# Kernel optimization log

Hardware: AMD Instinct MI355X
Metric: run time of the kernel (lower is better)

## Reference

```python
import jax, jax.numpy as jnp
import numpy as np

N_HEAD = 16
D_HEAD = 64
ROPE_BASE = 10000.0


def rotate_half(x):
    # interleaved pair rotation: (x0,x1,x2,x3,...) -> (-x1,x0,-x3,x2,...)
    x1 = x[..., ::2]
    x2 = x[..., 1::2]
    return jnp.stack((-x2, x1), axis=-1).reshape(x.shape)


def rope_tables(T, d_head, dtype):
    inv_freq = 1.0 / (ROPE_BASE ** (jnp.arange(0, d_head, 2, dtype=jnp.float32) / d_head))
    t = jnp.arange(T, dtype=jnp.float32)
    freqs = jnp.outer(t, inv_freq)                       # [T, d_head/2]
    emb = jnp.repeat(freqs, 2, axis=-1)                  # [T, d_head]
    return jnp.cos(emb).astype(dtype), jnp.sin(emb).astype(dtype)


def setup_inputs() -> dict:
    key = jax.random.key(0)
    k1, k2, k3 = jax.random.split(key, 3)
    B, T, D = 4, 2048, 1024
    x = jax.random.normal(k1, (B, T, D), dtype=jnp.float32)
    W_attn = jax.random.normal(k2, (D, 3 * D), dtype=jnp.float32) * 0.02
    W_proj = jax.random.normal(k3, (D, D), dtype=jnp.float32) * 0.02
    return {"x": x, "W_attn": W_attn, "W_proj": W_proj}


def reference(x, W_attn, W_proj):
    B, T, D = x.shape
    qkv = x @ W_attn                                      # [B, T, 3D]
    qkv = qkv.reshape(B, T, 3, N_HEAD, D_HEAD).transpose(2, 0, 3, 1, 4)
    q, k, v = qkv[0], qkv[1], qkv[2]                      # [B, H, T, d]

    cos, sin = rope_tables(T, D_HEAD, q.dtype)            # [T, d]
    q = q * cos + rotate_half(q) * sin
    k = k * cos + rotate_half(k) * sin

    scale = 1.0 / jnp.sqrt(jnp.asarray(D_HEAD, dtype=q.dtype))
    att = jnp.einsum('bhqd,bhkd->bhqk', q, k) * scale     # [B, H, T, T]
    causal = jnp.tril(jnp.ones((T, T), dtype=bool))
    att = jnp.where(causal, att, jnp.asarray(-jnp.inf, dtype=att.dtype))
    att = jax.nn.softmax(att, axis=-1)
    y = jnp.einsum('bhqk,bhkd->bhqd', att, v)             # [B, H, T, d]
    y = y.transpose(0, 2, 1, 3).reshape(B, T, D)
    return y @ W_proj
```

## Files before the change

### kernel.cpp

```cpp
#include <hip/hip_runtime.h>
#include <hip/hip_bf16.h>

typedef unsigned short ushort_t;
typedef __attribute__((ext_vector_type(8))) short bf16x8;
typedef __attribute__((ext_vector_type(4))) float f32x4;
typedef __attribute__((ext_vector_type(4))) unsigned short u16x4;

#define DEVI __device__ __forceinline__

#define WAITVM(N) asm volatile("s_waitcnt vmcnt(" #N ")" ::: "memory")
DEVI void bar_raw() { asm volatile("s_barrier" ::: "memory"); }

DEVI ushort_t f2bf(float f) {
  __hip_bfloat16 h = __float2bfloat16(f);
  return __builtin_bit_cast(unsigned short, h);
}

typedef const __attribute__((address_space(1))) void gvoid_t;
typedef __attribute__((address_space(3))) void lvoid_t;

DEVI void gload_lds16(const void* g, void* l) {
  __builtin_amdgcn_global_load_lds((gvoid_t*)g, (lvoid_t*)l, 16, 0, 0);
}

DEVI f32x4 mfma16(bf16x8 a, bf16x8 b, f32x4 c) {
  return __builtin_amdgcn_mfma_f32_16x16x32_bf16(a, b, c, 0, 0, 0);
}

DEVI bf16x8 lds_frag(const ushort_t* base, int row, int k) {
  int ch = (k >> 3) ^ (row & 7);
  return *(const bf16x8*)(base + row * 64 + ch * 8);
}

template <int ROWS>
DEVI void stage_swz(const ushort_t* src, int ld, ushort_t* lds, int wid, int lane) {
#pragma unroll
  for (int i = 0; i < ROWS / 32; ++i) {
    int r = i * 32 + wid * 8 + (lane >> 3);
    int p = lane & 7;
    int cl = p ^ (r & 7);
    gload_lds16(src + (size_t)r * ld + cl * 8, lds + r * 64 + p * 8);
  }
}


__global__ void k_convert(const float* __restrict__ in, ushort_t* __restrict__ out) {
  int i = blockIdx.x * 256 + threadIdx.x;
  float4 v = ((const float4*)in)[i];
  u16x4 o = {f2bf(v.x), f2bf(v.y), f2bf(v.z), f2bf(v.w)};
  ((u16x4*)out)[i] = o;
}

__global__ void k_transpose(const float* __restrict__ in, ushort_t* __restrict__ out,
                            int R, int C) {
  __shared__ ushort_t tile[64][65];
  int r0 = blockIdx.y * 64, c0 = blockIdx.x * 64;
  int t = threadIdx.x;
  int tc = t & 63, tr = t >> 6;
#pragma unroll
  for (int i = 0; i < 16; ++i) {
    int r = i * 4 + tr;
    tile[r][tc] = f2bf(in[(size_t)(r0 + r) * C + c0 + tc]);
  }
  __syncthreads();
#pragma unroll
  for (int i = 0; i < 16; ++i) {
    int c = i * 4 + tr;
    out[(size_t)(c0 + c) * R + r0 + tc] = tile[tc][c];
  }
}

__global__ void k_rope_tab(float* __restrict__ ct, float* __restrict__ st) {
  int idx = blockIdx.x * 256 + threadIdx.x;
  int t = idx >> 5, i = idx & 31;
  float inv = powf(10000.0f, -(float)(2 * i) * (1.0f / 64.0f));
  float fr = (float)t * inv;
  ct[idx] = cosf(fr);
  st[idx] = sinf(fr);
}


__global__ __launch_bounds__(256, 2) void k_gemm_qkv(
    const ushort_t* __restrict__ A, const ushort_t* __restrict__ Bt,
    const float* __restrict__ ct, const float* __restrict__ st,
    ushort_t* __restrict__ Qo, ushort_t* __restrict__ Ko, ushort_t* __restrict__ Vto) {
  __shared__ ushort_t sA[2][128 * 64];
  __shared__ ushort_t sB[2][128 * 64];
  int bid = blockIdx.x;
  int swz = (bid & 7) * 192 + (bid >> 3);
  int bm = swz / 24, bn = swz - bm * 24;
  int wid = threadIdx.x >> 6, lane = threadIdx.x & 63;
  int wm = wid >> 1, wn = wid & 1;
  const ushort_t* Abase = A + (size_t)bm * 128 * 1024;
  const ushort_t* Bbase = Bt + (size_t)bn * 128 * 1024;
  f32x4 acc[4][4] = {};
  stage_swz<128>(Abase, 1024, sA[0], wid, lane);
  stage_swz<128>(Bbase, 1024, sB[0], wid, lane);
  for (int kt = 0; kt < 16; ++kt) {
    int cur = kt & 1;
    if (kt < 15) {
      stage_swz<128>(Abase + (kt + 1) * 64, 1024, sA[cur ^ 1], wid, lane);
      stage_swz<128>(Bbase + (kt + 1) * 64, 1024, sB[cur ^ 1], wid, lane);
      WAITVM(8);
    } else {
      WAITVM(0);
    }
    bar_raw();
#pragma unroll
    for (int kk = 0; kk < 2; ++kk) {
      bf16x8 af[4], bfr[4];
#pragma unroll
      for (int mt = 0; mt < 4; ++mt)
        af[mt] = lds_frag(sA[cur], wm * 64 + mt * 16 + (lane & 15), kk * 32 + (lane >> 4) * 8);
#pragma unroll
      for (int nt = 0; nt < 4; ++nt)
        bfr[nt] = lds_frag(sB[cur], wn * 64 + nt * 16 + (lane & 15), kk * 32 + (lane >> 4) * 8);
#pragma unroll
      for (int mt = 0; mt < 4; ++mt)
#pragma unroll
        for (int nt = 0; nt < 4; ++nt) acc[mt][nt] = mfma16(af[mt], bfr[nt], acc[mt][nt]);
    }
    bar_raw();
  }
  int gm0 = bm * 128 + wm * 64;
  int gn0 = bn * 128 + wn * 64;
#pragma unroll
  for (int mt = 0; mt < 4; ++mt) {
#pragma unroll
    for (int nt = 0; nt < 4; ++nt) {
      f32x4 v = acc[mt][nt];
      int n = gn0 + nt * 16 + (lane & 15);
      int sidx = n >> 10, h = (n >> 6) & 15, d = n & 63;
      if (sidx == 2) {
        int m0r = gm0 + mt * 16 + (lane >> 4) * 4;
        int b = m0r >> 11, tpos = m0r & 2047;
        u16x4 pk = {f2bf(v[0]), f2bf(v[1]), f2bf(v[2]), f2bf(v[3])};
        *(u16x4*)(Vto + (((size_t)b * 16 + h) * 64 + d) * 2048 + tpos) = pk;
      } else {
        ushort_t* dst = (sidx == 0) ? Qo : Ko;
#pragma unroll
        for (int r = 0; r < 4; ++r) {
          float x = v[r];
          float px = __shfl_xor(x, 1);
          int m = gm0 + mt * 16 + (lane >> 4) * 4 + r;
          int b = m >> 11, tpos = m & 2047;
          float c = ct[tpos * 32 + (d >> 1)];
          float s = st[tpos * 32 + (d >> 1)];
          float val = (d & 1) ? (x * c + px * s) : (x * c - px * s);
          if (sidx == 0) val *= 0.18033688011112042f;
          dst[(((size_t)b * 16 + h) * 2048 + tpos) * 64 + d] = f2bf(val);
        }
      }
    }
  }
}


__global__ __launch_bounds__(256, 2) void k_attn(
    const ushort_t* __restrict__ Qg, const ushort_t* __restrict__ Kg,
    const ushort_t* __restrict__ Vtg, ushort_t* __restrict__ Yg) {
  __shared__ ushort_t sK[2][64 * 64];
  __shared__ ushort_t sV[2][64 * 64];
  __shared__ ushort_t sP[4][2][32 * 64];
  int bid = blockIdx.x;
  int wid = threadIdx.x >> 6, lane = threadIdx.x & 63;
  int bh = (bid & 7) * 8 + ((bid >> 3) & 7);
  int ps = bid >> 6;
  const ushort_t* Qb = Qg + (size_t)bh * (2048 * 64);
  const ushort_t* Kb = Kg + (size_t)bh * (2048 * 64);
  const ushort_t* Vb = Vtg + (size_t)bh * (64 * 2048);
  int b = bh >> 4, h = bh & 15;
  const bf16x8 ones = {0x3F80, 0x3F80, 0x3F80, 0x3F80, 0x3F80, 0x3F80, 0x3F80, 0x3F80};

  for (int t = 0; t < 2; ++t) {
    int qs = t ? (15 - ps) : ps;
    int q0 = qs * 128;
    int qw = q0 + wid * 32;
    int jmaxb = (q0 + 127) >> 6;
    int jmaxw = (qw + 31) >> 6;
    bf16x8 qf[2][2];
#pragma unroll
    for (int mt = 0; mt < 2; ++mt)
#pragma unroll
      for (int kk = 0; kk < 2; ++kk)
        qf[mt][kk] = *(const bf16x8*)(Qb + (size_t)(qw + mt * 16 + (lane & 15)) * 64 +
                                      kk * 32 + (lane >> 4) * 8);
    f32x4 o[2][4] = {};
    f32x4 l[2] = {};
    stage_swz<64>(Kb, 64, sK[0], wid, lane);
    stage_swz<64>(Vb, 2048, sV[0], wid, lane);
    for (int j = 0; j <= jmaxb; ++j) {
      int cur = j & 1;
      if (j < jmaxb) {
        stage_swz<64>(Kb + (size_t)(j + 1) * 64 * 64, 64, sK[cur ^ 1], wid, lane);
        stage_swz<64>(Vb + (j + 1) * 64, 2048, sV[cur ^ 1], wid, lane);
        WAITVM(4);
      } else {
        WAITVM(0);
      }
      bar_raw();
      if (j <= jmaxw) {
        ushort_t* sPw = sP[wid][cur];
        f32x4 st[2][4] = {};
#pragma unroll
        for (int kk = 0; kk < 2; ++kk) {
          bf16x8 kf[4];
#pragma unroll
          for (int nt = 0; nt < 4; ++nt)
            kf[nt] = lds_frag(sK[cur], nt * 16 + (lane & 15), kk * 32 + (lane >> 4) * 8);
#pragma unroll
          for (int mt = 0; mt < 2; ++mt)
#pragma unroll
            for (int nt = 0; nt < 4; ++nt)
              st[mt][nt] = mfma16(kf[nt], qf[mt][kk], st[mt][nt]);
        }
        if (j == jmaxw) {
#pragma unroll
          for (int mt = 0; mt < 2; ++mt)
#pragma unroll
            for (int nt = 0; nt < 4; ++nt)
#pragma unroll
              for (int r = 0; r < 4; ++r) {
                int kv = j * 64 + nt * 16 + (lane >> 4) * 4 + r;
                int q = qw + mt * 16 + (lane & 15);
                if (kv > q) st[mt][nt][r] = -1e30f;
              }
        }
        int g = lane >> 4;
#pragma unroll
        for (int mt = 0; mt < 2; ++mt) {
          int row = mt * 16 + (lane & 15);
#pragma unroll
          for (int nt = 0; nt < 4; ++nt) {
            u16x4 pk = {f2bf(__builtin_amdgcn_exp2f(st[mt][nt][0])),
                        f2bf(__builtin_amdgcn_exp2f(st[mt][nt][1])),
                        f2bf(__builtin_amdgcn_exp2f(st[mt][nt][2])),
                        f2bf(__builtin_amdgcn_exp2f(st[mt][nt][3]))};
            int ch = (nt * 2 + (g >> 1)) ^ (row & 7);
            *(u16x4*)(sPw + row * 64 + ch * 8 + (g & 1) * 4) = pk;
          }
        }
#pragma unroll
        for (int kk = 0; kk < 2; ++kk) {
          bf16x8 pf[2], vf[4];
#pragma unroll
          for (int mt = 0; mt < 2; ++mt)
            pf[mt] = lds_frag(sPw, mt * 16 + (lane & 15), kk * 32 + (lane >> 4) * 8);
#pragma unroll
          for (int dt = 0; dt < 4; ++dt)
            vf[dt] = lds_frag(sV[cur], dt * 16 + (lane & 15), kk * 32 + (lane >> 4) * 8);
#pragma unroll
          for (int mt = 0; mt < 2; ++mt) {
#pragma unroll
            for (int dt = 0; dt < 4; ++dt) o[mt][dt] = mfma16(pf[mt], vf[dt], o[mt][dt]);
            l[mt] = mfma16(pf[mt], ones, l[mt]);
          }
        }
      }
      bar_raw();
    }
#pragma unroll
    for (int mt = 0; mt < 2; ++mt)
#pragma unroll
      for (int r = 0; r < 4; ++r) {
        float inv = 1.0f / l[mt][r];
        int q = qw + mt * 16 + (lane >> 4) * 4 + r;
#pragma unroll
        for (int dt = 0; dt < 4; ++dt) {
          int d = dt * 16 + (lane & 15);
          Yg[((size_t)b * 2048 + q) * 1024 + h * 64 + d] = f2bf(o[mt][dt][r] * inv);
        }
      }
  }
}


__global__ __launch_bounds__(256, 2) void k_gemm_proj(
    const ushort_t* __restrict__ A, const ushort_t* __restrict__ Bt,
    float* __restrict__ out) {
  __shared__ ushort_t sA[2][128 * 64];
  __shared__ ushort_t sB[2][128 * 64];
  int bid = blockIdx.x;
  int swz = (bid & 7) * 64 + (bid >> 3);
  int bm = swz >> 3, bn = swz & 7;
  int wid = threadIdx.x >> 6, lane = threadIdx.x & 63;
  int wm = wid >> 1, wn = wid & 1;
  const ushort_t* Abase = A + (size_t)bm * 128 * 1024;
  const ushort_t* Bbase = Bt + (size_t)bn * 128 * 1024;
  f32x4 acc[4][4] = {};
  stage_swz<128>(Abase, 1024, sA[0], wid, lane);
  stage_swz<128>(Bbase, 1024, sB[0], wid, lane);
  for (int kt = 0; kt < 16; ++kt) {
    int cur = kt & 1;
    if (kt < 15) {
      stage_swz<128>(Abase + (kt + 1) * 64, 1024, sA[cur ^ 1], wid, lane);
      stage_swz<128>(Bbase + (kt + 1) * 64, 1024, sB[cur ^ 1], wid, lane);
      WAITVM(8);
    } else {
      WAITVM(0);
    }
    bar_raw();
#pragma unroll
    for (int kk = 0; kk < 2; ++kk) {
      bf16x8 af[4], bfr[4];
#pragma unroll
      for (int mt = 0; mt < 4; ++mt)
        af[mt] = lds_frag(sA[cur], wm * 64 + mt * 16 + (lane & 15), kk * 32 + (lane >> 4) * 8);
#pragma unroll
      for (int nt = 0; nt < 4; ++nt)
        bfr[nt] = lds_frag(sB[cur], wn * 64 + nt * 16 + (lane & 15), kk * 32 + (lane >> 4) * 8);
#pragma unroll
      for (int mt = 0; mt < 4; ++mt)
#pragma unroll
        for (int nt = 0; nt < 4; ++nt) acc[mt][nt] = mfma16(af[mt], bfr[nt], acc[mt][nt]);
    }
    bar_raw();
  }
  int gm0 = bm * 128 + wm * 64;
  int gn0 = bn * 128 + wn * 64;
#pragma unroll
  for (int mt = 0; mt < 4; ++mt)
#pragma unroll
    for (int nt = 0; nt < 4; ++nt) {
      f32x4 v = acc[mt][nt];
      int n = gn0 + nt * 16 + (lane & 15);
#pragma unroll
      for (int r = 0; r < 4; ++r) {
        int m = gm0 + mt * 16 + (lane >> 4) * 4 + r;
        out[(size_t)m * 1024 + n] = v[r];
      }
    }
}


extern "C" void kernel_launch(void* const* d_in, const int* in_sizes, int n_in,
                              void* d_out, int out_size, void* d_ws, size_t ws_size,
                              hipStream_t stream) {
  (void)in_sizes; (void)n_in; (void)out_size; (void)ws_size;
  const float* x  = (const float*)d_in[0];
  const float* Wa = (const float*)d_in[1];
  const float* Wp = (const float*)d_in[2];
  float* out = (float*)d_out;
  char* ws = (char*)d_ws;

  ushort_t* xb   = (ushort_t*)(ws + 0);
  ushort_t* WaT  = (ushort_t*)(ws + 16777216);
  ushort_t* WpT  = (ushort_t*)(ws + 23068672);
  float*    ctab = (float*)   (ws + 25165824);
  float*    stab = (float*)   (ws + 25427968);
  ushort_t* Qb   = (ushort_t*)(ws + 25690112);
  ushort_t* Kb   = (ushort_t*)(ws + 42467328);
  ushort_t* Vtb  = (ushort_t*)(ws + 59244544);

  k_convert<<<8192, 256, 0, stream>>>(x, xb);
  k_transpose<<<dim3(48, 16), 256, 0, stream>>>(Wa, WaT, 1024, 3072);
  k_transpose<<<dim3(16, 16), 256, 0, stream>>>(Wp, WpT, 1024, 1024);
  k_rope_tab<<<256, 256, 0, stream>>>(ctab, stab);
  k_gemm_qkv<<<1536, 256, 0, stream>>>(xb, WaT, ctab, stab, Qb, Kb, Vtb);
  k_attn<<<512, 256, 0, stream>>>(Qb, Kb, Vtb, xb);
  k_gemm_proj<<<512, 256, 0, stream>>>(xb, WpT, out);
}
```

Baseline: 159.7 us.

## Enlarge GEMM tiles to 512-thread blocks and prioritize MFMA waves in attention

The QKV GEMM grows from 128x128 to 256x256 tiles with 8 waves, and the projection GEMM goes to 256x128 tiles with 512 threads, so each staged tile feeds more MFMAs and global traffic per FLOP drops. The staging helper is generalized to any thread count. The attention kernel raises wave priority around its MFMA sections with s_setprio. The larger tiles use 64KB (QKV) and 48KB (projection) of LDS plus more accumulators per thread, which may lower occupancy. The grids also shrink to 384 and 256 blocks, which may underfill the 256 CUs.

```diff
diff --git a/kernel.cpp b/kernel.cpp
--- a/kernel.cpp
+++ b/kernel.cpp
@@ -32,12 +32,12 @@
   return *(const bf16x8*)(base + row * 64 + ch * 8);
 }
 
-template <int ROWS>
-DEVI void stage_swz(const ushort_t* src, int ld, ushort_t* lds, int wid, int lane) {
-#pragma unroll
-  for (int i = 0; i < ROWS / 32; ++i) {
-    int r = i * 32 + wid * 8 + (lane >> 3);
-    int p = lane & 7;
+template <int ROWS, int THR>
+DEVI void stage_swz(const ushort_t* src, int ld, ushort_t* lds, int tid) {
+#pragma unroll
+  for (int i = 0; i < ROWS / (THR / 8); ++i) {
+    int r = i * (THR / 8) + (tid >> 3);
+    int p = tid & 7;
     int cl = p ^ (r & 7);
     gload_lds16(src + (size_t)r * ld + cl * 8, lds + r * 64 + p * 8);
   }
@@ -80,27 +80,28 @@
 }
 
 
-__global__ __launch_bounds__(256, 2) void k_gemm_qkv(
+__global__ __launch_bounds__(512, 2) void k_gemm_qkv(
     const ushort_t* __restrict__ A, const ushort_t* __restrict__ Bt,
     const float* __restrict__ ct, const float* __restrict__ st,
     ushort_t* __restrict__ Qo, ushort_t* __restrict__ Ko, ushort_t* __restrict__ Vto) {
-  __shared__ ushort_t sA[2][128 * 64];
-  __shared__ ushort_t sB[2][128 * 64];
+  __shared__ ushort_t sA[2][256 * 64];
+  __shared__ ushort_t sB[2][256 * 64];
+  int tid = threadIdx.x;
   int bid = blockIdx.x;
-  int swz = (bid & 7) * 192 + (bid >> 3);
-  int bm = swz / 24, bn = swz - bm * 24;
-  int wid = threadIdx.x >> 6, lane = threadIdx.x & 63;
-  int wm = wid >> 1, wn = wid & 1;
-  const ushort_t* Abase = A + (size_t)bm * 128 * 1024;
-  const ushort_t* Bbase = Bt + (size_t)bn * 128 * 1024;
-  f32x4 acc[4][4] = {};
-  stage_swz<128>(Abase, 1024, sA[0], wid, lane);
-  stage_swz<128>(Bbase, 1024, sB[0], wid, lane);
+  int swz = (bid & 7) * 48 + (bid >> 3);
+  int bm = swz / 12, bn = swz % 12;
+  int lane = tid & 63;
+  int wm = (tid >> 6) >> 2, wn = (tid >> 6) & 3;
+  const ushort_t* Abase = A + (size_t)bm * 256 * 1024;
+  const ushort_t* Bbase = Bt + (size_t)bn * 256 * 1024;
+  f32x4 acc[8][4] = {};
+  stage_swz<256, 512>(Abase, 1024, sA[0], tid);
+  stage_swz<256, 512>(Bbase, 1024, sB[0], tid);
   for (int kt = 0; kt < 16; ++kt) {
     int cur = kt & 1;
     if (kt < 15) {
-      stage_swz<128>(Abase + (kt + 1) * 64, 1024, sA[cur ^ 1], wid, lane);
-      stage_swz<128>(Bbase + (kt + 1) * 64, 1024, sB[cur ^ 1], wid, lane);
+      stage_swz<256, 512>(Abase + (kt + 1) * 64, 1024, sA[cur ^ 1], tid);
+      stage_swz<256, 512>(Bbase + (kt + 1) * 64, 1024, sB[cur ^ 1], tid);
       WAITVM(8);
     } else {
       WAITVM(0);
@@ -108,24 +109,24 @@
     bar_raw();
 #pragma unroll
     for (int kk = 0; kk < 2; ++kk) {
-      bf16x8 af[4], bfr[4];
-#pragma unroll
-      for (int mt = 0; mt < 4; ++mt)
-        af[mt] = lds_frag(sA[cur], wm * 64 + mt * 16 + (lane & 15), kk * 32 + (lane >> 4) * 8);
+      bf16x8 af[8], bfr[4];
+#pragma unroll
+      for (int mt = 0; mt < 8; ++mt)
+        af[mt] = lds_frag(sA[cur], wm * 128 + mt * 16 + (lane & 15), kk * 32 + (lane >> 4) * 8);
 #pragma unroll
       for (int nt = 0; nt < 4; ++nt)
         bfr[nt] = lds_frag(sB[cur], wn * 64 + nt * 16 + (lane & 15), kk * 32 + (lane >> 4) * 8);
 #pragma unroll
-      for (int mt = 0; mt < 4; ++mt)
+      for (int mt = 0; mt < 8; ++mt)
 #pragma unroll
         for (int nt = 0; nt < 4; ++nt) acc[mt][nt] = mfma16(af[mt], bfr[nt], acc[mt][nt]);
     }
     bar_raw();
   }
-  int gm0 = bm * 128 + wm * 64;
-  int gn0 = bn * 128 + wn * 64;
-#pragma unroll
-  for (int mt = 0; mt < 4; ++mt) {
+  int gm0 = bm * 256 + wm * 128;
+  int gn0 = bn * 256 + wn * 64;
+#pragma unroll
+  for (int mt = 0; mt < 8; ++mt) {
 #pragma unroll
     for (int nt = 0; nt < 4; ++nt) {
       f32x4 v = acc[mt][nt];
@@ -163,7 +164,8 @@
   __shared__ ushort_t sV[2][64 * 64];
   __shared__ ushort_t sP[4][2][32 * 64];
   int bid = blockIdx.x;
-  int wid = threadIdx.x >> 6, lane = threadIdx.x & 63;
+  int tid = threadIdx.x;
+  int wid = tid >> 6, lane = tid & 63;
   int bh = (bid & 7) * 8 + ((bid >> 3) & 7);
   int ps = bid >> 6;
   const ushort_t* Qb = Qg + (size_t)bh * (2048 * 64);
@@ -187,13 +189,13 @@
                                       kk * 32 + (lane >> 4) * 8);
     f32x4 o[2][4] = {};
     f32x4 l[2] = {};
-    stage_swz<64>(Kb, 64, sK[0], wid, lane);
-    stage_swz<64>(Vb, 2048, sV[0], wid, lane);
+    stage_swz<64, 256>(Kb, 64, sK[0], tid);
+    stage_swz<64, 256>(Vb, 2048, sV[0], tid);
     for (int j = 0; j <= jmaxb; ++j) {
       int cur = j & 1;
       if (j < jmaxb) {
-        stage_swz<64>(Kb + (size_t)(j + 1) * 64 * 64, 64, sK[cur ^ 1], wid, lane);
-        stage_swz<64>(Vb + (j + 1) * 64, 2048, sV[cur ^ 1], wid, lane);
+        stage_swz<64, 256>(Kb + (size_t)(j + 1) * 64 * 64, 64, sK[cur ^ 1], tid);
+        stage_swz<64, 256>(Vb + (j + 1) * 64, 2048, sV[cur ^ 1], tid);
         WAITVM(4);
       } else {
         WAITVM(0);
@@ -202,6 +204,7 @@
       if (j <= jmaxw) {
         ushort_t* sPw = sP[wid][cur];
         f32x4 st[2][4] = {};
+        __builtin_amdgcn_s_setprio(1);
 #pragma unroll
         for (int kk = 0; kk < 2; ++kk) {
           bf16x8 kf[4];
@@ -214,6 +217,7 @@
             for (int nt = 0; nt < 4; ++nt)
               st[mt][nt] = mfma16(kf[nt], qf[mt][kk], st[mt][nt]);
         }
+        __builtin_amdgcn_s_setprio(0);
         if (j == jmaxw) {
 #pragma unroll
           for (int mt = 0; mt < 2; ++mt)
@@ -240,6 +244,7 @@
             *(u16x4*)(sPw + row * 64 + ch * 8 + (g & 1) * 4) = pk;
           }
         }
+        __builtin_amdgcn_s_setprio(1);
 #pragma unroll
         for (int kk = 0; kk < 2; ++kk) {
           bf16x8 pf[2], vf[4];
@@ -256,6 +261,7 @@
             l[mt] = mfma16(pf[mt], ones, l[mt]);
           }
         }
+        __builtin_amdgcn_s_setprio(0);
       }
       bar_raw();
     }
@@ -275,53 +281,54 @@
 }
 
 
-__global__ __launch_bounds__(256, 2) void k_gemm_proj(
+__global__ __launch_bounds__(512, 2) void k_gemm_proj(
     const ushort_t* __restrict__ A, const ushort_t* __restrict__ Bt,
     float* __restrict__ out) {
-  __shared__ ushort_t sA[2][128 * 64];
+  __shared__ ushort_t sA[2][256 * 64];
   __shared__ ushort_t sB[2][128 * 64];
+  int tid = threadIdx.x;
   int bid = blockIdx.x;
-  int swz = (bid & 7) * 64 + (bid >> 3);
+  int swz = (bid & 7) * 32 + (bid >> 3);
   int bm = swz >> 3, bn = swz & 7;
-  int wid = threadIdx.x >> 6, lane = threadIdx.x & 63;
-  int wm = wid >> 1, wn = wid & 1;
-  const ushort_t* Abase = A + (size_t)bm * 128 * 1024;
+  int lane = tid & 63;
+  int wm = (tid >> 6) >> 2, wn = (tid >> 6) & 3;
+  const ushort_t* Abase = A + (size_t)bm * 256 * 1024;
   const ushort_t* Bbase = Bt + (size_t)bn * 128 * 1024;
-  f32x4 acc[4][4] = {};
-  stage_swz<128>(Abase, 1024, sA[0], wid, lane);
-  stage_swz<128>(Bbase, 1024, sB[0], wid, lane);
+  f32x4 acc[8][2] = {};
+  stage_swz<256, 512>(Abase, 1024, sA[0], tid);
+  stage_swz<128, 512>(Bbase, 1024, sB[0], tid);
   for (int kt = 0; kt < 16; ++kt) {
     int cur = kt & 1;
     if (kt < 15) {
-      stage_swz<128>(Abase + (kt + 1) * 64, 1024, sA[cur ^ 1], wid, lane);
-      stage_swz<128>(Bbase + (kt + 1) * 64, 1024, sB[cur ^ 1], wid, lane);
-      WAITVM(8);
+      stage_swz<256, 512>(Abase + (kt + 1) * 64, 1024, sA[cur ^ 1], tid);
+      stage_swz<128, 512>(Bbase + (kt + 1) * 64, 1024, sB[cur ^ 1], tid);
+      WAITVM(6);
     } else {
       WAITVM(0);
     }
     bar_raw();
 #pragma unroll
     for (int kk = 0; kk < 2; ++kk) {
-      bf16x8 af[4], bfr[4];
-#pragma unroll
-      for (int mt = 0; mt < 4; ++mt)
-        af[mt] = lds_frag(sA[cur], wm * 64 + mt * 16 + (lane & 15), kk * 32 + (lane >> 4) * 8);
-#pragma unroll
-      for (int nt = 0; nt < 4; ++nt)
-        bfr[nt] = lds_frag(sB[cur], wn * 64 + nt * 16 + (lane & 15), kk * 32 + (lane >> 4) * 8);
-#pragma unroll
-      for (int mt = 0; mt < 4; ++mt)
-#pragma unroll
-        for (int nt = 0; nt < 4; ++nt) acc[mt][nt] = mfma16(af[mt], bfr[nt], acc[mt][nt]);
+      bf16x8 af[8], bfr[2];
+#pragma unroll
+      for (int mt = 0; mt < 8; ++mt)
+        af[mt] = lds_frag(sA[cur], wm * 128 + mt * 16 + (lane & 15), kk * 32 + (lane >> 4) * 8);
+#pragma unroll
+      for (int nt = 0; nt < 2; ++nt)
+        bfr[nt] = lds_frag(sB[cur], wn * 32 + nt * 16 + (lane & 15), kk * 32 + (lane >> 4) * 8);
+#pragma unroll
+      for (int mt = 0; mt < 8; ++mt)
+#pragma unroll
+        for (int nt = 0; nt < 2; ++nt) acc[mt][nt] = mfma16(af[mt], bfr[nt], acc[mt][nt]);
     }
     bar_raw();
   }
-  int gm0 = bm * 128 + wm * 64;
-  int gn0 = bn * 128 + wn * 64;
-#pragma unroll
-  for (int mt = 0; mt < 4; ++mt)
-#pragma unroll
-    for (int nt = 0; nt < 4; ++nt) {
+  int gm0 = bm * 256 + wm * 128;
+  int gn0 = bn * 128 + wn * 32;
+#pragma unroll
+  for (int mt = 0; mt < 8; ++mt)
+#pragma unroll
+    for (int nt = 0; nt < 2; ++nt) {
       f32x4 v = acc[mt][nt];
       int n = gn0 + nt * 16 + (lane & 15);
 #pragma unroll
@@ -356,7 +363,7 @@
   k_transpose<<<dim3(48, 16), 256, 0, stream>>>(Wa, WaT, 1024, 3072);
   k_transpose<<<dim3(16, 16), 256, 0, stream>>>(Wp, WpT, 1024, 1024);
   k_rope_tab<<<256, 256, 0, stream>>>(ctab, stab);
-  k_gemm_qkv<<<1536, 256, 0, stream>>>(xb, WaT, ctab, stab, Qb, Kb, Vtb);
+  k_gemm_qkv<<<384, 512, 0, stream>>>(xb, WaT, ctab, stab, Qb, Kb, Vtb);
   k_attn<<<512, 256, 0, stream>>>(Qb, Kb, Vtb, xb);
-  k_gemm_proj<<<512, 256, 0, stream>>>(xb, WpT, out);
-}
+  k_gemm_proj<<<256, 512, 0, stream>>>(xb, WpT, out);
+}
```

New measurement: 170.8 us. +7.0%, slower.
